# Performance work log

Measured on AMD Instinct MI355X. Metric: run time of the kernel, lower is better.

Reference implementation:

```python
import jax, jax.numpy as jnp
import numpy as np

B, M, H, D, K, V = 32, 4096, 32, 4096, 128, 128

def setup_inputs() -> dict:
    key = jax.random.key(0)
    ks = jax.random.split(key, 7)
    s = lambda fan: 1.0 / np.sqrt(fan)
    return {
        "x": jax.random.normal(ks[0], (B, D), jnp.float32),
        "K_prev": jax.random.normal(ks[1], (B, M, K), jnp.float32),
        "V_prev": jax.random.normal(ks[2], (B, M, V), jnp.float32),
        "P_q": jax.random.normal(ks[3], (H, D, K), jnp.float32) * s(D),
        "P_k": jax.random.normal(ks[4], (D, K), jnp.float32) * s(D),
        "P_v": jax.random.normal(ks[5], (D, V), jnp.float32) * s(D),
        "P_o": jax.random.normal(ks[6], (H, D, V), jnp.float32) * s(D),
    }

def reference(x, K_prev, V_prev, P_q, P_k, P_v, P_o):
    # per-head query projection: [b,d] x [h,d,k] -> [b,h,k]
    q = jnp.einsum('bd,hdk->bhk', x, P_q)
    # shared (multi-query) K/V projection of the new token, appended to cache
    k_new = jnp.einsum('bd,dk->bk', x, P_k)          # [b,k]
    v_new = jnp.einsum('bd,dv->bv', x, P_v)          # [b,v]
    K_new = jnp.concatenate([K_prev, k_new[:, None, :]], axis=1)  # [b,m+1,k]
    V_new = jnp.concatenate([V_prev, v_new[:, None, :]], axis=1)  # [b,m+1,v]
    # attention over shared cache
    logits = jnp.einsum('bhk,bmk->bhm', q, K_new)    # [b,h,m+1]
    w = jax.nn.softmax(logits, axis=-1)
    o = jnp.einsum('bhm,bmv->bhv', w, V_new)         # [b,h,v]
    y = jnp.einsum('bhv,hdv->bd', o, P_o)            # [b,d]
    return (y, K_new, V_new)
```

## Files before the change

### kernel.cpp

```cpp
#include <hip/hip_runtime.h>

#define B_ 32
#define M_ 4096
#define M1_ 4097
#define H_ 32
#define D_ 4096

typedef float float4_ __attribute__((ext_vector_type(4)));
typedef float f32x4 __attribute__((ext_vector_type(4)));
typedef short short8 __attribute__((ext_vector_type(8)));
typedef short short4_ __attribute__((ext_vector_type(4)));

#define KOFF 131072
#define VOFF 16912384

#define Q_OFF     0u
#define O_OFF     139264u
#define YPART_OFF 270336u
#define QPART_OFF 1318912u
#define APO_OFF   1318912u
#define MSUM_OFF  5775360u

#define WAITV(n) asm volatile("s_waitcnt vmcnt(" #n ")" ::: "memory")
#define SBAR() __builtin_amdgcn_sched_barrier(0)

__device__ __forceinline__ unsigned short f2bf(float f) {
  union { float f; unsigned u; } cv; cv.f = f;
  return (unsigned short)((cv.u + 0x7FFFu + ((cv.u >> 16) & 1u)) >> 16);
}
__device__ __forceinline__ float bf2f(unsigned short b) {
  union { unsigned u; float f; } cv; cv.u = ((unsigned)b) << 16;
  return cv.f;
}
__device__ __forceinline__ short8 pack8(const float* t) {
  short8 r;
#pragma unroll
  for (int j = 0; j < 8; ++j) r[j] = (short)f2bf(t[j]);
  return r;
}
__device__ __forceinline__ short8 load8cvt(const float* __restrict__ p) {
  float t[8];
  float4_ v0 = *(const float4_*)p;
  float4_ v1 = *(const float4_*)(p + 4);
#pragma unroll
  for (int j = 0; j < 4; ++j) { t[j] = v0[j]; t[4 + j] = v1[j]; }
  return pack8(t);
}
__device__ __forceinline__ void load_lds16(const float* g, float* l) {
  __builtin_amdgcn_global_load_lds(
      (const __attribute__((address_space(1))) unsigned int*)g,
      (__attribute__((address_space(3))) unsigned int*)l, 16, 0, 0);
}

__global__ __launch_bounds__(256) void k_proj(const float* __restrict__ x,
    const float* __restrict__ Pq, const float* __restrict__ Pk,
    const float* __restrict__ Pv, float* __restrict__ qpart)
{
  int bid = blockIdx.x;
  int hh = bid >> 5;
  int c  = bid & 31;
  const float* W = (hh < 32) ? (Pq + (size_t)hh * D_ * 128)
                             : ((hh == 32) ? Pk : Pv);
  int d0 = c * 128;
  int tid = threadIdx.x;
  int w = tid >> 6, l = tid & 63, l15 = l & 15, lg = l >> 4;
  f32x4 acc[2][2] = {};
  for (int ks = 0; ks < 4; ++ks) {
    int dk = d0 + ks * 32 + lg * 8;
    short8 af[2];
#pragma unroll
    for (int bt = 0; bt < 2; ++bt)
      af[bt] = load8cvt(x + (size_t)(bt * 16 + l15) * D_ + dk);
    short8 bf[2];
#pragma unroll
    for (int nti = 0; nti < 2; ++nti) {
      int col = (2 * w + nti) * 16 + l15;
      float t[8];
#pragma unroll
      for (int j = 0; j < 8; ++j) t[j] = W[(size_t)(dk + j) * 128 + col];
      bf[nti] = pack8(t);
    }
#pragma unroll
    for (int bt = 0; bt < 2; ++bt)
#pragma unroll
      for (int nti = 0; nti < 2; ++nti)
        acc[bt][nti] = __builtin_amdgcn_mfma_f32_16x16x32_bf16(af[bt], bf[nti], acc[bt][nti], 0, 0, 0);
  }
#pragma unroll
  for (int bt = 0; bt < 2; ++bt)
#pragma unroll
    for (int nti = 0; nti < 2; ++nti) {
      int k = (2 * w + nti) * 16 + l15;
#pragma unroll
      for (int i = 0; i < 4; ++i) {
        int b = bt * 16 + lg * 4 + i;
        qpart[(size_t)((c * 34 + hh) * 32 + b) * 128 + k] = acc[bt][nti][i];
      }
    }
}

__global__ __launch_bounds__(256) void k_reduce_q(const float* __restrict__ qpart,
    float* __restrict__ q, float* __restrict__ dout)
{
  int idx = blockIdx.x * 256 + threadIdx.x;
  if (idx >= 34 * 32 * 128) return;
  float s = 0.f;
#pragma unroll
  for (int cc = 0; cc < 32; ++cc) s += qpart[(size_t)cc * 139264 + idx];
  q[idx] = s;
  int hh = idx >> 12;
  if (hh >= 32) {
    int b = (idx >> 7) & 31, k = idx & 127;
    size_t off = (hh == 32) ? (size_t)KOFF : (size_t)VOFF;
    dout[off + ((size_t)b * M1_ + M_) * 128 + k] = s;
  }
}

#define ISSUE(T, KR, VB) do { \
  const float* Kc_ = Kb + (T) * 16 * 128; \
  const float* Vc_ = Vb + (T) * 16 * 128; \
  const float* Krow_ = Kc_ + (size_t)l15 * 128; \
  _Pragma("unroll") \
  for (int ks = 0; ks < 4; ++ks) { \
    KR[2 * ks]     = *(const float4_*)(Krow_ + ks * 32 + lg * 8); \
    KR[2 * ks + 1] = *(const float4_*)(Krow_ + ks * 32 + lg * 8 + 4); \
  } \
  _Pragma("unroll") \
  for (int i = 0; i < 8; ++i) load_lds16(Vc_ + i * 256 + l * 4, VB + i * 256); \
} while (0)

#define DO_CHUNK(T, KR, VB) do { \
   \
  float* Knrow_ = Knb + (T) * 16 * 128 + (size_t)l15 * 128; \
  _Pragma("unroll") \
  for (int ks = 0; ks < 4; ++ks) { \
    *(float4_*)(Knrow_ + ks * 32 + lg * 8)     = KR[2 * ks]; \
    *(float4_*)(Knrow_ + ks * 32 + lg * 8 + 4) = KR[2 * ks + 1]; \
  } \
   \
  float* Vnc_ = Vnb + (T) * 16 * 128; \
  _Pragma("unroll") \
  for (int i = 0; i < 8; ++i) { \
    float4_ t_ = *(const float4_*)(VB + (i * 64 + l) * 4); \
    *(float4_*)(Vnc_ + (size_t)(i * 64 + l) * 4) = t_; \
  } \
   \
  short8 kf_[4]; \
  _Pragma("unroll") \
  for (int ks = 0; ks < 4; ++ks) { \
    float tt_[8]; \
    _Pragma("unroll") \
    for (int j = 0; j < 4; ++j) { tt_[j] = KR[2 * ks][j]; tt_[4 + j] = KR[2 * ks + 1][j]; } \
    kf_[ks] = pack8(tt_); \
  } \
   \
  f32x4 sacc_[2] = {}; \
  _Pragma("unroll") \
  for (int ks = 0; ks < 4; ++ks) \
    _Pragma("unroll") \
    for (int ht = 0; ht < 2; ++ht) \
      sacc_[ht] = __builtin_amdgcn_mfma_f32_16x16x32_bf16(af[ht][ks], kf_[ks], sacc_[ht], 0, 0, 0); \
   \
  _Pragma("unroll") \
  for (int ht = 0; ht < 2; ++ht) { \
    f32x4 mx_; \
    _Pragma("unroll") \
    for (int i = 0; i < 4; ++i) { \
      float v_ = sacc_[ht][i]; \
      v_ = fmaxf(v_, __shfl_xor(v_, 1)); v_ = fmaxf(v_, __shfl_xor(v_, 2)); \
      v_ = fmaxf(v_, __shfl_xor(v_, 4)); v_ = fmaxf(v_, __shfl_xor(v_, 8)); \
      mx_[i] = v_; \
    } \
    f32x4 fsc_; \
    _Pragma("unroll") \
    for (int i = 0; i < 4; ++i) { \
      float mn_ = fmaxf(mrun[ht][i], mx_[i]); \
      fsc_[i] = __expf(mrun[ht][i] - mn_); \
      mrun[ht][i] = mn_; \
    } \
    _Pragma("unroll") \
    for (int vt = 0; vt < 8; ++vt) oacc[ht][vt] *= fsc_; \
    _Pragma("unroll") \
    for (int i = 0; i < 4; ++i) { \
      float p_ = __expf(sacc_[ht][i] - mrun[ht][i]); \
      lsum[ht][i] = lsum[ht][i] * fsc_[i] + p_; \
      Plds[w][ht * 16 + lg * 4 + i][l15] = f2bf(p_); \
    } \
  } \
  asm volatile("" ::: "memory"); \
   \
  short8 z_ = {}; \
  short8 pa_[2]; \
  _Pragma("unroll") \
  for (int ht = 0; ht < 2; ++ht) \
    pa_[ht] = (lg < 2) ? *(const short8*)&Plds[w][ht * 16 + l15][lg * 8] : z_; \
  _Pragma("unroll") \
  for (int vt = 0; vt < 8; ++vt) { \
    short8 bfv_ = z_; \
    if (lg < 2) { \
      float t_[8]; \
      _Pragma("unroll") \
      for (int j = 0; j < 8; ++j) t_[j] = VB[(lg * 8 + j) * 128 + vt * 16 + l15]; \
      bfv_ = pack8(t_); \
    } \
    _Pragma("unroll") \
    for (int ht = 0; ht < 2; ++ht) \
      oacc[ht][vt] = __builtin_amdgcn_mfma_f32_16x16x32_bf16(pa_[ht], bfv_, oacc[ht][vt], 0, 0, 0); \
  } \
} while (0)

__global__ __launch_bounds__(256, 2) void k_attn(const float* __restrict__ Kp,
    const float* __restrict__ Vp, const float* __restrict__ q,
    float* __restrict__ dout, unsigned short* __restrict__ apo,
    float* __restrict__ msum)
{
  __shared__ float Vbuf[4][2][2048];
  __shared__ unsigned short Plds[4][32][16];
  int bid = blockIdx.x;
  int b = bid >> 4;
  int tid = threadIdx.x, w = tid >> 6, l = tid & 63, l15 = l & 15, lg = l >> 4;
  int wid = (bid & 15) * 4 + w;
  const float* Kb = Kp + ((size_t)b * M_ + wid * 64) * 128;
  const float* Vb = Vp + ((size_t)b * M_ + wid * 64) * 128;
  float* Knb = dout + KOFF + ((size_t)b * M1_ + wid * 64) * 128;
  float* Vnb = dout + VOFF + ((size_t)b * M1_ + wid * 64) * 128;
  float* vb0 = &Vbuf[w][0][0];
  float* vb1 = &Vbuf[w][1][0];

  short8 af[2][4];
#pragma unroll
  for (int ks = 0; ks < 4; ++ks)
#pragma unroll
    for (int ht = 0; ht < 2; ++ht)
      af[ht][ks] = load8cvt(q + (size_t)((ht * 16 + l15) * 32 + b) * 128 + ks * 32 + lg * 8);

  float4_ krA[8], krB[8];
  f32x4 mrun[2], lsum[2], oacc[2][8];
#pragma unroll
  for (int ht = 0; ht < 2; ++ht) {
#pragma unroll
    for (int i = 0; i < 4; ++i) { mrun[ht][i] = -3e38f; lsum[ht][i] = 0.f; }
#pragma unroll
    for (int vt = 0; vt < 8; ++vt) oacc[ht][vt] = f32x4{0.f, 0.f, 0.f, 0.f};
  }

  ISSUE(0, krA, vb0); SBAR();
  ISSUE(1, krB, vb1); SBAR();
  WAITV(16); SBAR();
  DO_CHUNK(0, krA, vb0);
  ISSUE(2, krA, vb0); SBAR();
  WAITV(32); SBAR();
  DO_CHUNK(1, krB, vb1);
  ISSUE(3, krB, vb1); SBAR();
  WAITV(32); SBAR();
  DO_CHUNK(2, krA, vb0);
  WAITV(16); SBAR();
  DO_CHUNK(3, krB, vb1);

#pragma unroll
  for (int ht = 0; ht < 2; ++ht)
#pragma unroll
    for (int i = 0; i < 4; ++i) {
      float s = lsum[ht][i];
      s += __shfl_xor(s, 1); s += __shfl_xor(s, 2);
      s += __shfl_xor(s, 4); s += __shfl_xor(s, 8);
      lsum[ht][i] = s;
    }
  size_t slot = (size_t)(b * 64 + wid) * 32;
  if (l15 == 0) {
#pragma unroll
    for (int ht = 0; ht < 2; ++ht)
#pragma unroll
      for (int i = 0; i < 4; ++i) {
        int h = ht * 16 + lg * 4 + i;
        msum[(slot + h) * 2]     = mrun[ht][i];
        msum[(slot + h) * 2 + 1] = lsum[ht][i];
      }
  }
#pragma unroll
  for (int ht = 0; ht < 2; ++ht)
#pragma unroll
    for (int vt = 0; vt < 8; ++vt)
#pragma unroll
      for (int i = 0; i < 4; ++i) {
        int h = ht * 16 + lg * 4 + i;
        int v = vt * 16 + l15;
        apo[(slot + h) * 128 + v] = f2bf(oacc[ht][vt][i]);
      }
}

__global__ __launch_bounds__(256) void k_combine(const unsigned short* __restrict__ apo,
    const float* __restrict__ msum, const float* __restrict__ q, float* __restrict__ o)
{
  __shared__ float redN[4][128];
  __shared__ float redD[4];
  int bid = blockIdx.x;
  int b = bid >> 5, h = bid & 31;
  int tid = threadIdx.x, w = tid >> 6, l = tid & 63;

  const float* qh = q + (size_t)(h * 32 + b) * 128;
  const float* kn = q + (size_t)(1024 + b) * 128;
  const float* vn = q + (size_t)(1056 + b) * 128;
  float e = qh[2 * l] * kn[2 * l] + qh[2 * l + 1] * kn[2 * l + 1];
#pragma unroll
  for (int d = 1; d < 64; d <<= 1) e += __shfl_xor(e, d);

  float gm = msum[((size_t)(b * 64 + l) * 32 + h) * 2];
#pragma unroll
  for (int d = 1; d < 64; d <<= 1) gm = fmaxf(gm, __shfl_xor(gm, d));
  gm = fmaxf(gm, e);
  float pe = __expf(e - gm);

  float num0 = 0.f, num1 = 0.f, den = 0.f;
#pragma unroll 4
  for (int i = 0; i < 16; ++i) {
    int cc = w * 16 + i;
    size_t slot = (size_t)(b * 64 + cc) * 32 + h;
    float sc = __expf(msum[slot * 2] - gm);
    den += sc * msum[slot * 2 + 1];
    unsigned pp = *(const unsigned*)&apo[slot * 128 + l * 2];
    num0 += sc * bf2f((unsigned short)(pp & 0xFFFFu));
    num1 += sc * bf2f((unsigned short)(pp >> 16));
  }
  redN[w][l * 2] = num0;
  redN[w][l * 2 + 1] = num1;
  if (l == 0) redD[w] = den + (w == 0 ? pe : 0.f);
  __syncthreads();
  if (tid < 128) {
    float num = redN[0][tid] + redN[1][tid] + redN[2][tid] + redN[3][tid] + pe * vn[tid];
    float dd  = redD[0] + redD[1] + redD[2] + redD[3];
    o[((size_t)(b * 32 + h)) * 128 + tid] = num / dd;
  }
}

__global__ __launch_bounds__(256) void k_out(const float* __restrict__ o,
    const float* __restrict__ Po, float* __restrict__ ypart)
{
  int bid = blockIdx.x;
  int dt = bid >> 3, hg = bid & 7;
  int tid = threadIdx.x, w = tid >> 6, l = tid & 63, l15 = l & 15, lg = l >> 4;
  int d = dt * 64 + w * 16 + l15;
  f32x4 acc[2] = {};
  for (int hi = 0; hi < 4; ++hi) {
    int h = hg * 4 + hi;
#pragma unroll
    for (int ks = 0; ks < 4; ++ks) {
      short8 af[2];
#pragma unroll
      for (int bt = 0; bt < 2; ++bt)
        af[bt] = load8cvt(o + ((size_t)((bt * 16 + l15) * 32 + h)) * 128 + ks * 32 + lg * 8);
      short8 bf = load8cvt(Po + ((size_t)h * D_ + d) * 128 + ks * 32 + lg * 8);
#pragma unroll
      for (int bt = 0; bt < 2; ++bt)
        acc[bt] = __builtin_amdgcn_mfma_f32_16x16x32_bf16(af[bt], bf, acc[bt], 0, 0, 0);
    }
  }
#pragma unroll
  for (int bt = 0; bt < 2; ++bt)
#pragma unroll
    for (int i = 0; i < 4; ++i) {
      int b = bt * 16 + lg * 4 + i;
      ypart[((size_t)(hg * 32 + b)) * 4096 + d] = acc[bt][i];
    }
}

__global__ __launch_bounds__(256) void k_reduce_y(const float* __restrict__ ypart,
    float* __restrict__ dout)
{
  int idx = blockIdx.x * 256 + threadIdx.x;
  float s = 0.f;
#pragma unroll
  for (int g = 0; g < 8; ++g) s += ypart[(size_t)g * 131072 + idx];
  dout[idx] = s;
}

extern "C" void kernel_launch(void* const* d_in, const int* in_sizes, int n_in,
                              void* d_out, int out_size, void* d_ws, size_t ws_size,
                              hipStream_t stream) {
  (void)in_sizes; (void)n_in; (void)out_size; (void)ws_size;
  const float* x  = (const float*)d_in[0];
  const float* Kp = (const float*)d_in[1];
  const float* Vp = (const float*)d_in[2];
  const float* Pq = (const float*)d_in[3];
  const float* Pk = (const float*)d_in[4];
  const float* Pv = (const float*)d_in[5];
  const float* Po = (const float*)d_in[6];
  float* out = (float*)d_out;
  float* ws  = (float*)d_ws;
  float* q     = ws + Q_OFF;
  float* o     = ws + O_OFF;
  float* ypart = ws + YPART_OFF;
  float* qpart = ws + QPART_OFF;
  unsigned short* apo = (unsigned short*)(ws + APO_OFF);
  float* msum  = ws + MSUM_OFF;

  hipLaunchKernelGGL(k_proj,     dim3(1088), dim3(256), 0, stream, x, Pq, Pk, Pv, qpart);
  hipLaunchKernelGGL(k_reduce_q, dim3(544),  dim3(256), 0, stream, qpart, q, out);
  hipLaunchKernelGGL(k_attn,     dim3(512),  dim3(256), 0, stream, Kp, Vp, q, out, apo, msum);
  hipLaunchKernelGGL(k_combine,  dim3(1024), dim3(256), 0, stream, apo, msum, q, o);
  hipLaunchKernelGGL(k_out,      dim3(512),  dim3(256), 0, stream, o, Po, ypart);
  hipLaunchKernelGGL(k_reduce_y, dim3(512),  dim3(256), 0, stream, ypart, out);
}
```

Before: 135.0 us.

## Store q partials in bf16 and pre-combine per-block attention partials in LDS

Projection partial sums are now written as bf16 instead of fp32, halving workspace traffic between the projection and reduce kernels. The attention kernel merges its four waves' softmax partials (max, sum, rescaled outputs) through shared memory before writing, so each block emits one partial per head instead of four. This shrinks the apo/msum workspace and the combine kernel's reads by a factor of four. The cost is an extra block-wide reduction with two barriers, and bf16 rounding of the q partials before they are summed, which adds error.

```diff
diff --git a/kernel.cpp b/kernel.cpp
--- a/kernel.cpp
+++ b/kernel.cpp
@@ -19,7 +19,7 @@
 #define YPART_OFF 270336u
 #define QPART_OFF 1318912u
 #define APO_OFF   1318912u
-#define MSUM_OFF  5775360u
+#define MSUM_OFF  2367488u
 
 #define WAITV(n) asm volatile("s_waitcnt vmcnt(" #n ")" ::: "memory")
 #define SBAR() __builtin_amdgcn_sched_barrier(0)
@@ -54,7 +54,7 @@
 
 __global__ __launch_bounds__(256) void k_proj(const float* __restrict__ x,
     const float* __restrict__ Pq, const float* __restrict__ Pk,
-    const float* __restrict__ Pv, float* __restrict__ qpart)
+    const float* __restrict__ Pv, unsigned short* __restrict__ qpart)
 {
   int bid = blockIdx.x;
   int hh = bid >> 5;
@@ -94,19 +94,19 @@
 #pragma unroll
       for (int i = 0; i < 4; ++i) {
         int b = bt * 16 + lg * 4 + i;
-        qpart[(size_t)((c * 34 + hh) * 32 + b) * 128 + k] = acc[bt][nti][i];
+        qpart[(size_t)((c * 34 + hh) * 32 + b) * 128 + k] = f2bf(acc[bt][nti][i]);
       }
     }
 }
 
-__global__ __launch_bounds__(256) void k_reduce_q(const float* __restrict__ qpart,
+__global__ __launch_bounds__(256) void k_reduce_q(const unsigned short* __restrict__ qpart,
     float* __restrict__ q, float* __restrict__ dout)
 {
   int idx = blockIdx.x * 256 + threadIdx.x;
   if (idx >= 34 * 32 * 128) return;
   float s = 0.f;
 #pragma unroll
-  for (int cc = 0; cc < 32; ++cc) s += qpart[(size_t)cc * 139264 + idx];
+  for (int cc = 0; cc < 32; ++cc) s += bf2f(qpart[(size_t)cc * 139264 + idx]);
   q[idx] = s;
   int hh = idx >> 12;
   if (hh >= 32) {
@@ -216,6 +216,7 @@
 {
   __shared__ float Vbuf[4][2][2048];
   __shared__ unsigned short Plds[4][32][16];
+  __shared__ float Mh[4][32], Sh[4][32];
   int bid = blockIdx.x;
   int b = bid >> 4;
   int tid = threadIdx.x, w = tid >> 6, l = tid & 63, l15 = l & 15, lg = l >> 4;
@@ -266,27 +267,45 @@
       s += __shfl_xor(s, 4); s += __shfl_xor(s, 8);
       lsum[ht][i] = s;
     }
-  size_t slot = (size_t)(b * 64 + wid) * 32;
   if (l15 == 0) {
 #pragma unroll
     for (int ht = 0; ht < 2; ++ht)
 #pragma unroll
       for (int i = 0; i < 4; ++i) {
         int h = ht * 16 + lg * 4 + i;
-        msum[(slot + h) * 2]     = mrun[ht][i];
-        msum[(slot + h) * 2 + 1] = lsum[ht][i];
+        Mh[w][h] = mrun[ht][i];
+        Sh[w][h] = lsum[ht][i];
       }
   }
+  __syncthreads();
+  float* Ob = &Vbuf[w][0][0];
 #pragma unroll
   for (int ht = 0; ht < 2; ++ht)
 #pragma unroll
-    for (int vt = 0; vt < 8; ++vt)
-#pragma unroll
-      for (int i = 0; i < 4; ++i) {
-        int h = ht * 16 + lg * 4 + i;
-        int v = vt * 16 + l15;
-        apo[(slot + h) * 128 + v] = f2bf(oacc[ht][vt][i]);
-      }
+    for (int i = 0; i < 4; ++i) {
+      int h = ht * 16 + lg * 4 + i;
+      float ms = fmaxf(fmaxf(Mh[0][h], Mh[1][h]), fmaxf(Mh[2][h], Mh[3][h]));
+      float f = __expf(mrun[ht][i] - ms);
+#pragma unroll
+      for (int vt = 0; vt < 8; ++vt)
+        Ob[h * 128 + vt * 16 + l15] = oacc[ht][vt][i] * f;
+    }
+  __syncthreads();
+  int blk = bid & 15;
+  size_t sblk = ((size_t)b * 16 + blk) * 32;
+  if (tid < 32) {
+    int h = tid;
+    float ms = fmaxf(fmaxf(Mh[0][h], Mh[1][h]), fmaxf(Mh[2][h], Mh[3][h]));
+    float ss = Sh[0][h] * __expf(Mh[0][h] - ms) + Sh[1][h] * __expf(Mh[1][h] - ms)
+             + Sh[2][h] * __expf(Mh[2][h] - ms) + Sh[3][h] * __expf(Mh[3][h] - ms);
+    msum[(sblk + h) * 2]     = ms;
+    msum[(sblk + h) * 2 + 1] = ss;
+  }
+  const float* Vall = &Vbuf[0][0][0];
+  for (int idx = tid; idx < 4096; idx += 256) {
+    float s = Vall[idx] + Vall[4096 + idx] + Vall[8192 + idx] + Vall[12288 + idx];
+    apo[(sblk + (idx >> 7)) * 128 + (idx & 127)] = f2bf(s);
+  }
 }
 
 __global__ __launch_bounds__(256) void k_combine(const unsigned short* __restrict__ apo,
@@ -305,17 +324,17 @@
 #pragma unroll
   for (int d = 1; d < 64; d <<= 1) e += __shfl_xor(e, d);
 
-  float gm = msum[((size_t)(b * 64 + l) * 32 + h) * 2];
+  float gm = (l < 16) ? msum[((size_t)(b * 16 + l) * 32 + h) * 2] : -3e38f;
 #pragma unroll
   for (int d = 1; d < 64; d <<= 1) gm = fmaxf(gm, __shfl_xor(gm, d));
   gm = fmaxf(gm, e);
   float pe = __expf(e - gm);
 
   float num0 = 0.f, num1 = 0.f, den = 0.f;
-#pragma unroll 4
-  for (int i = 0; i < 16; ++i) {
-    int cc = w * 16 + i;
-    size_t slot = (size_t)(b * 64 + cc) * 32 + h;
+#pragma unroll
+  for (int i = 0; i < 4; ++i) {
+    int cc = w * 4 + i;
+    size_t slot = (size_t)(b * 16 + cc) * 32 + h;
     float sc = __expf(msum[slot * 2] - gm);
     den += sc * msum[slot * 2 + 1];
     unsigned pp = *(const unsigned*)&apo[slot * 128 + l * 2];
@@ -390,8 +409,8 @@
   float* q     = ws + Q_OFF;
   float* o     = ws + O_OFF;
   float* ypart = ws + YPART_OFF;
-  float* qpart = ws + QPART_OFF;
-  unsigned short* apo = (unsigned short*)(ws + APO_OFF);
+  unsigned short* qpart = (unsigned short*)(ws + QPART_OFF);
+  unsigned short* apo   = (unsigned short*)(ws + APO_OFF);
   float* msum  = ws + MSUM_OFF;
 
   hipLaunchKernelGGL(k_proj,     dim3(1088), dim3(256), 0, stream, x, Pq, Pk, Pv, qpart);
```

Measured after the change: 127.4 us. 5.6% less time.
